# Optimization experiments

Measured on AMD Instinct MI355X. Metric: run time of the kernel, lower is better.

## Reference

```python
import jax, jax.numpy as jnp
import numpy as np

B, Hh, Ww, C = 32, 56, 56, 256
WIN, SHIFT, HEADS = 7, 3, 8
N = WIN * WIN
nW = (Hh // WIN) * (Ww // WIN)


def _rel_pos_index(w):
    coords = np.stack(np.meshgrid(np.arange(w), np.arange(w), indexing='ij'))  # (2,w,w)
    flat = coords.reshape(2, -1)
    rel = (flat[:, :, None] - flat[:, None, :]).transpose(1, 2, 0)  # (N,N,2)
    rel[..., 0] += w - 1
    rel[..., 1] += w - 1
    rel[..., 0] *= 2 * w - 1
    return rel.sum(-1)  # (N,N) int


def _shift_attn_mask(H, W, w, s):
    img = np.zeros((H, W))
    cnt = 0
    for hs in (slice(0, -w), slice(-w, -s), slice(-s, None)):
        for ws in (slice(0, -w), slice(-w, -s), slice(-s, None)):
            img[hs, ws] = cnt
            cnt += 1
    mw = img.reshape(H // w, w, W // w, w).transpose(0, 2, 1, 3).reshape(-1, w * w)  # (nW,N)
    diff = mw[:, None, :] - mw[:, :, None]
    return np.where(diff != 0, -100.0, 0.0).astype(np.float32)  # (nW,N,N)


REL_IDX = jnp.asarray(_rel_pos_index(WIN))


def layer_norm(x, g, b):
    m = x.mean(-1, keepdims=True)
    v = ((x - m) ** 2).mean(-1, keepdims=True)
    return (x - m) / jnp.sqrt(v + 1e-5) * g + b


def setup_inputs() -> dict:
    key = jax.random.key(0)
    ks = jax.random.split(key, 10)
    s02 = 0.02
    x = jax.random.normal(ks[0], (B, Hh * Ww, C), jnp.float32)
    qkv_w = jax.random.normal(ks[1], (3 * C, C), jnp.float32) * s02
    qkv_b = jnp.zeros((3 * C,), jnp.float32)
    rpb_table = jax.random.normal(ks[2], ((2 * WIN - 1) ** 2, HEADS), jnp.float32) * s02
    proj_w = jax.random.normal(ks[3], (C, C), jnp.float32) * s02
    proj_b = jnp.zeros((C,), jnp.float32)
    fc1_w = jax.random.normal(ks[4], (4 * C, C), jnp.float32) * s02
    fc1_b = jnp.zeros((4 * C,), jnp.float32)
    fc2_w = jax.random.normal(ks[5], (C, 4 * C), jnp.float32) * s02
    fc2_b = jnp.zeros((C,), jnp.float32)
    attn_mask = jnp.asarray(_shift_attn_mask(Hh, Ww, WIN, SHIFT))
    # saliency masks: per-token binary fg/bg -> additive 0/-100 key masks
    fg_tok = jax.random.bernoulli(ks[6], 0.5, (B * nW, N))
    sal_fg = jnp.where(fg_tok[:, None, :], 0.0, -100.0) * jnp.ones((1, N, 1), jnp.float32)
    sal_bg = jnp.where(fg_tok[:, None, :], -100.0, 0.0) * jnp.ones((1, N, 1), jnp.float32)
    return dict(x=x, qkv_w=qkv_w, qkv_b=qkv_b, rpb_table=rpb_table, proj_w=proj_w,
                proj_b=proj_b, norm1_g=jnp.ones((C,)), norm1_b=jnp.zeros((C,)),
                norm2_g=jnp.ones((C,)), norm2_b=jnp.zeros((C,)),
                fc1_w=fc1_w, fc1_b=fc1_b, fc2_w=fc2_w, fc2_b=fc2_b,
                attn_mask=attn_mask, sal_fg_attn_mask=sal_fg.astype(jnp.float32),
                sal_bg_attn_mask=sal_bg.astype(jnp.float32))


def reference(x, qkv_w, qkv_b, rpb_table, proj_w, proj_b, norm1_g, norm1_b,
              norm2_g, norm2_b, fc1_w, fc1_b, fc2_w, fc2_b,
              attn_mask, sal_fg_attn_mask, sal_bg_attn_mask):
    Bb, L, Cc = x.shape
    d = Cc // HEADS
    scale = d ** -0.5
    shortcut = x
    xn = layer_norm(x, norm1_g, norm1_b).reshape(Bb, Hh, Ww, Cc)
    xs = jnp.roll(xn, (-SHIFT, -SHIFT), axis=(1, 2))
    # window partition -> (B*nW, N, C)
    nh = Hh // WIN
    xw = xs.reshape(Bb, nh, WIN, nh, WIN, Cc).transpose(0, 1, 3, 2, 4, 5).reshape(-1, N, Cc)
    B_ = xw.shape[0]
    qkv = (xw @ qkv_w.T + qkv_b).reshape(B_, N, 3, HEADS, d).transpose(2, 0, 3, 1, 4)
    q, k, v = qkv[0] * scale, qkv[1], qkv[2]  # (B_, h, N, d)
    attn = jnp.einsum('bhnd,bhmd->bhnm', q, k)
    rpb = rpb_table[REL_IDX.reshape(-1)].reshape(N, N, HEADS).transpose(2, 0, 1)
    attn = attn + rpb[None]
    attn_fg = attn + sal_fg_attn_mask[:, None]
    attn_bg = attn + sal_bg_attn_mask[:, None]

    def add_shift(a):
        a = a.reshape(B_ // nW, nW, HEADS, N, N) + attn_mask[None, :, None]
        return a.reshape(B_, HEADS, N, N)

    p = jax.nn.softmax(add_shift(attn), axis=-1)
    p_fg = jax.nn.softmax(add_shift(attn_fg), axis=-1)
    p_bg = jax.nn.softmax(add_shift(attn_bg), axis=-1)
    o = jnp.einsum('bhnm,bhmd->bhnd', p + p_fg - p_bg, v)
    o = o.transpose(0, 2, 1, 3).reshape(B_, N, Cc)
    o = o @ proj_w.T + proj_b
    # window reverse + reverse shift
    xr = o.reshape(Bb, nh, nh, WIN, WIN, Cc).transpose(0, 1, 3, 2, 4, 5).reshape(Bb, Hh, Ww, Cc)
    xr = jnp.roll(xr, (SHIFT, SHIFT), axis=(1, 2)).reshape(Bb, L, Cc)
    x = shortcut + xr
    h = layer_norm(x, norm2_g, norm2_b)
    h = jax.nn.gelu(h @ fc1_w.T + fc1_b, approximate=False) @ fc2_w.T + fc2_b
    return x + h
```

## Files before the change

kernel.cpp:

```cpp
#include <hip/hip_runtime.h>
#include <hip/hip_bf16.h>

#define HH 56
#define WWD 56
#define WIN 7
#define SHIFT 3
#define HEADS 8
#define NTOK 49
#define NW 64
#define CDIM 256
#define DH 32
#define MROWS 100352
#define SCALE_Q 0.17677669529663687f

typedef float floatx4 __attribute__((ext_vector_type(4)));
typedef __bf16 bf16x8 __attribute__((ext_vector_type(8)));

__device__ __forceinline__ float wave_sum(float v) {
#pragma unroll
    for (int m = 1; m < 64; m <<= 1) v += __shfl_xor(v, m);
    return v;
}

__device__ __forceinline__ void glds16(const void* g, void* l) {
    __builtin_amdgcn_global_load_lds(
        (const __attribute__((address_space(1))) void*)g,
        (__attribute__((address_space(3))) void*)l, 16, 0, 0);
}

__global__ __launch_bounds__(256) void convert_weights_kernel(
    const float* __restrict__ qkv_w, const float* __restrict__ proj_w,
    const float* __restrict__ fc1_w, const float* __restrict__ fc2_w,
    __hip_bfloat16* __restrict__ dst)
{
    int i = blockIdx.x * 256 + threadIdx.x;
    float v;
    if (i < 196608)       v = qkv_w[i];
    else if (i < 262144)  v = proj_w[i - 196608];
    else if (i < 524288)  v = fc1_w[i - 262144];
    else                  v = fc2_w[i - 524288];
    dst[i] = __float2bfloat16(v);
}

template <bool SHIFTED>
__global__ __launch_bounds__(256) void ln_kernel(
    const float* __restrict__ x, const float* __restrict__ g,
    const float* __restrict__ bb, __hip_bfloat16* __restrict__ out)
{
    const int tok  = blockIdx.x * 4 + (threadIdx.x >> 6);
    const int lane = threadIdx.x & 63;
    const int c    = lane * 4;

    float4 v = *reinterpret_cast<const float4*>(x + (size_t)tok * CDIM + c);
    float s = v.x + v.y + v.z + v.w;
    s = wave_sum(s);
    const float mean = s * (1.0f / 256.0f);
    float d0 = v.x - mean, d1 = v.y - mean, d2 = v.z - mean, d3 = v.w - mean;
    float sq = d0 * d0 + d1 * d1 + d2 * d2 + d3 * d3;
    sq = wave_sum(sq);
    const float rstd = rsqrtf(sq * (1.0f / 256.0f) + 1e-5f);

    float4 gv = *reinterpret_cast<const float4*>(g + c);
    float4 bv = *reinterpret_cast<const float4*>(bb + c);

    union { __hip_bfloat16 h[4]; uint2 u; } pk;
    pk.h[0] = __float2bfloat16(d0 * rstd * gv.x + bv.x);
    pk.h[1] = __float2bfloat16(d1 * rstd * gv.y + bv.y);
    pk.h[2] = __float2bfloat16(d2 * rstd * gv.z + bv.z);
    pk.h[3] = __float2bfloat16(d3 * rstd * gv.w + bv.w);

    size_t oidx;
    if (SHIFTED) {
        int b = tok / 3136;
        int l = tok - b * 3136;
        int h = l / WWD, w = l - (l / WWD) * WWD;
        int hp = h - SHIFT; if (hp < 0) hp += HH;
        int wp = w - SHIFT; if (wp < 0) wp += WWD;
        int bwin = b * NW + (hp / WIN) * 8 + (wp / WIN);
        int n = (hp % WIN) * WIN + (wp % WIN);
        oidx = ((size_t)bwin * NTOK + n) * CDIM + c;
    } else {
        oidx = (size_t)tok * CDIM + c;
    }
    *reinterpret_cast<uint2*>(out + oidx) = pk.u;
}

template <int MODE>
__global__ __launch_bounds__(256) void gemm_kernel(
    const __hip_bfloat16* __restrict__ A,
    const __hip_bfloat16* __restrict__ Wt,
    const float* __restrict__ bias,
    void* __restrict__ outv,
    const float* __restrict__ aux,
    int M, int Nn, int K)
{
    __shared__ __hip_bfloat16 As[128 * 32];
    __shared__ __hip_bfloat16 Bs[128 * 32];

    const int t = threadIdx.x;
    const int wave = t >> 6, lane = t & 63;
    const int m0 = blockIdx.y * 128, n0 = blockIdx.x * 128;
    const int wr = (wave >> 1) * 64;
    const int wc = (wave & 1) * 64;

    floatx4 acc[4][4] = {};

    const int c0 = wave * 64 + lane;
    const int c1 = 256 + c0;
    const int r0 = c0 >> 2, p0 = c0 & 3, g0 = p0 ^ ((r0 >> 1) & 3);
    const int r1 = c1 >> 2, p1 = c1 & 3, g1 = p1 ^ ((r1 >> 1) & 3);
    const __hip_bfloat16* gA0 = A  + (size_t)(m0 + r0) * K + g0 * 8;
    const __hip_bfloat16* gA1 = A  + (size_t)(m0 + r1) * K + g1 * 8;
    const __hip_bfloat16* gB0 = Wt + (size_t)(n0 + r0) * K + g0 * 8;
    const __hip_bfloat16* gB1 = Wt + (size_t)(n0 + r1) * K + g1 * 8;
    const int base0 = (wave * 64) * 8;
    const int base1 = (256 + wave * 64) * 8;

    const int fm = lane & 15;
    const int g4 = lane >> 4;

    for (int k0 = 0; k0 < K; k0 += 32) {
        __syncthreads();
        glds16(gA0 + k0, As + base0);
        glds16(gA1 + k0, As + base1);
        glds16(gB0 + k0, Bs + base0);
        glds16(gB1 + k0, Bs + base1);
        __syncthreads();

        bf16x8 af[4], bfr[4];
#pragma unroll
        for (int mt = 0; mt < 4; ++mt) {
            const int ml = wr + mt * 16 + fm;
            af[mt] = *reinterpret_cast<const bf16x8*>(
                As + ml * 32 + ((g4 ^ ((ml >> 1) & 3)) * 8));
            const int nl = wc + mt * 16 + fm;
            bfr[mt] = *reinterpret_cast<const bf16x8*>(
                Bs + nl * 32 + ((g4 ^ ((nl >> 1) & 3)) * 8));
        }
#pragma unroll
        for (int mt = 0; mt < 4; ++mt)
#pragma unroll
            for (int nt = 0; nt < 4; ++nt)
                acc[mt][nt] = __builtin_amdgcn_mfma_f32_16x16x32_bf16(
                    af[mt], bfr[nt], acc[mt][nt], 0, 0, 0);
    }

    float bv[4];
#pragma unroll
    for (int nt = 0; nt < 4; ++nt) bv[nt] = bias[n0 + wc + nt * 16 + fm];

#pragma unroll
    for (int mt = 0; mt < 4; ++mt) {
#pragma unroll
        for (int r = 0; r < 4; ++r) {
            const int m_g = m0 + wr + mt * 16 + g4 * 4 + r;
            size_t row_idx = 0;
            if (MODE == 1) {
                int bwin = m_g / NTOK;
                int ntok = m_g - bwin * NTOK;
                int b = bwin >> 6, wi = bwin & 63;
                int rr = ntok / WIN, cc = ntok - rr * WIN;
                int hp = (wi >> 3) * WIN + rr;
                int wp = (wi & 7) * WIN + cc;
                int h = hp + SHIFT; if (h >= HH) h -= HH;
                int w = wp + SHIFT; if (w >= WWD) w -= WWD;
                row_idx = ((size_t)b * 3136 + h * WWD + w) * CDIM;
            }
#pragma unroll
            for (int nt = 0; nt < 4; ++nt) {
                const int n_g = n0 + wc + nt * 16 + fm;
                float val = acc[mt][nt][r] + bv[nt];
                if (MODE == 0) {
                    if (n_g < 256) val *= SCALE_Q;
                    reinterpret_cast<__hip_bfloat16*>(outv)[(size_t)m_g * Nn + n_g] =
                        __float2bfloat16(val);
                } else if (MODE == 2) {
                    float gl = 0.5f * val * (1.0f + erff(val * 0.70710678118654752f));
                    reinterpret_cast<__hip_bfloat16*>(outv)[(size_t)m_g * Nn + n_g] =
                        __float2bfloat16(gl);
                } else if (MODE == 3) {
                    size_t idx = (size_t)m_g * CDIM + n_g;
                    reinterpret_cast<float*>(outv)[idx] = aux[idx] + val;
                } else {
                    size_t idx = row_idx + n_g;
                    reinterpret_cast<float*>(outv)[idx] = aux[idx] + val;
                }
            }
        }
    }
}

__global__ __launch_bounds__(256) void attn_kernel(
    const __hip_bfloat16* __restrict__ qkv,
    const float* __restrict__ rpb_table,
    const float* __restrict__ sal_fg,
    __hip_bfloat16* __restrict__ o)
{
    __shared__ unsigned short Pl[4][64 * 64];
    __shared__ unsigned short Vt[4][32 * 64];
    __shared__ float rpb_l[4][172];

    const int t = threadIdx.x;
    const int wave = t >> 6, lane = t & 63;
    const int lane15 = lane & 15, g4 = lane >> 4;
    const int b_ = blockIdx.x >> 1;
    const int h = ((blockIdx.x & 1) << 2) | wave;

    unsigned short* Pw = Pl[wave];
    unsigned short* Vw = Vt[wave];
    float* rpbw = rpb_l[wave];

    const unsigned short* qkv_u = reinterpret_cast<const unsigned short*>(qkv);
    const size_t base = (size_t)b_ * (NTOK * 768) + h * DH;

#pragma unroll
    for (int it = 0; it < 32; ++it) {
        int idx = it * 64 + lane;
        int key = idx >> 5, d = idx & 31;
        unsigned short v = 0;
        if (key < NTOK) v = qkv_u[base + key * 768 + 512 + d];
        Vw[d * 64 + (((key >> 3) ^ (d & 7)) << 3) + (key & 7)] = v;
    }
#pragma unroll
    for (int it = 0; it < 3; ++it) {
        int i = it * 64 + lane;
        if (i < 169) rpbw[i] = rpb_table[i * 8 + h];
    }
    float sfv = (lane < NTOK) ? sal_fg[(size_t)b_ * (NTOK * NTOK) + lane] : -100.f;
    const unsigned long long fgmask = __ballot(sfv == 0.0f);

    bf16x8 kf[4], qf[4];
#pragma unroll
    for (int mt = 0; mt < 4; ++mt)
        kf[mt] = *reinterpret_cast<const bf16x8*>(
            qkv_u + base + (size_t)(mt * 16 + lane15) * 768 + 256 + g4 * 8);
#pragma unroll
    for (int nt = 0; nt < 4; ++nt)
        qf[nt] = *reinterpret_cast<const bf16x8*>(
            qkv_u + base + (size_t)(nt * 16 + lane15) * 768 + g4 * 8);

    floatx4 S[4][4] = {};
#pragma unroll
    for (int mt = 0; mt < 4; ++mt)
#pragma unroll
        for (int nt = 0; nt < 4; ++nt)
            S[mt][nt] = __builtin_amdgcn_mfma_f32_16x16x32_bf16(
                kf[mt], qf[nt], S[mt][nt], 0, 0, 0);

    const int wr_ = (b_ & 63) >> 3, wc_ = (b_ & 63) & 7;
    int qlin[4], qreg[4];
#pragma unroll
    for (int nt = 0; nt < 4; ++nt) {
        int q = nt * 16 + lane15;
        int qr = (q * 147) >> 10, qc = q - qr * 7;
        qlin[nt] = q + 6 * qr + 84;
        qreg[nt] = ((wr_ == 7) ? ((qr < 4) ? 1 : 2) : 0) * 3
                 + ((wc_ == 7) ? ((qc < 4) ? 1 : 2) : 0);
    }

#pragma unroll
    for (int mt = 0; mt < 4; ++mt)
#pragma unroll
        for (int r = 0; r < 4; ++r) {
            int key = mt * 16 + g4 * 4 + r;
            int kr = (key * 147) >> 10, kc = key - kr * 7;
            int klin = key + 6 * kr;
            int kreg = ((wr_ == 7) ? ((kr < 4) ? 1 : 2) : 0) * 3
                     + ((wc_ == 7) ? ((kc < 4) ? 1 : 2) : 0);
            bool pad = key >= NTOK;
#pragma unroll
            for (int nt = 0; nt < 4; ++nt) {
                int idx = qlin[nt] - klin;
                idx = idx < 0 ? 0 : (idx > 168 ? 168 : idx);
                float s = S[mt][nt][r] + rpbw[idx]
                        + ((qreg[nt] == kreg) ? 0.f : -100.f);
                S[mt][nt][r] = pad ? -1e30f : s;
            }
        }

    float M0[4], M1[4], M2[4], R0[4], R1[4], R2[4];
#pragma unroll
    for (int nt = 0; nt < 4; ++nt) {
        float a0 = -1e30f, a1 = -1e30f, a2 = -1e30f;
#pragma unroll
        for (int mt = 0; mt < 4; ++mt)
#pragma unroll
            for (int r = 0; r < 4; ++r) {
                int key = mt * 16 + g4 * 4 + r;
                float sf = ((fgmask >> key) & 1ULL) ? 0.f : -100.f;
                float s = S[mt][nt][r];
                a0 = fmaxf(a0, s);
                a1 = fmaxf(a1, s + sf);
                a2 = fmaxf(a2, s - 100.f - sf);
            }
        a0 = fmaxf(a0, __shfl_xor(a0, 16)); a0 = fmaxf(a0, __shfl_xor(a0, 32));
        a1 = fmaxf(a1, __shfl_xor(a1, 16)); a1 = fmaxf(a1, __shfl_xor(a1, 32));
        a2 = fmaxf(a2, __shfl_xor(a2, 16)); a2 = fmaxf(a2, __shfl_xor(a2, 32));
        float s0 = 0.f, s1 = 0.f, s2 = 0.f;
#pragma unroll
        for (int mt = 0; mt < 4; ++mt)
#pragma unroll
            for (int r = 0; r < 4; ++r) {
                int key = mt * 16 + g4 * 4 + r;
                float sf = ((fgmask >> key) & 1ULL) ? 0.f : -100.f;
                float s = S[mt][nt][r];
                s0 += __expf(s - a0);
                s1 += __expf(s + sf - a1);
                s2 += __expf(s - 100.f - sf - a2);
            }
        s0 += __shfl_xor(s0, 16); s0 += __shfl_xor(s0, 32);
        s1 += __shfl_xor(s1, 16); s1 += __shfl_xor(s1, 32);
        s2 += __shfl_xor(s2, 16); s2 += __shfl_xor(s2, 32);
        M0[nt] = a0; M1[nt] = a1; M2[nt] = a2;
        R0[nt] = 1.f / s0; R1[nt] = 1.f / s1; R2[nt] = 1.f / s2;
    }

#pragma unroll
    for (int mt = 0; mt < 4; ++mt)
#pragma unroll
        for (int rp = 0; rp < 2; ++rp) {
            int key0 = mt * 16 + g4 * 4 + 2 * rp;
            float sf0 = ((fgmask >> key0) & 1ULL) ? 0.f : -100.f;
            float sf1 = ((fgmask >> (key0 + 1)) & 1ULL) ? 0.f : -100.f;
            int chunk = key0 >> 3;
#pragma unroll
            for (int nt = 0; nt < 4; ++nt) {
                float sA = S[mt][nt][2 * rp];
                float sB = S[mt][nt][2 * rp + 1];
                float pA = __expf(sA - M0[nt]) * R0[nt]
                         + __expf(sA + sf0 - M1[nt]) * R1[nt]
                         - __expf(sA - 100.f - sf0 - M2[nt]) * R2[nt];
                float pB = __expf(sB - M0[nt]) * R0[nt]
                         + __expf(sB + sf1 - M1[nt]) * R1[nt]
                         - __expf(sB - 100.f - sf1 - M2[nt]) * R2[nt];
                union { __hip_bfloat16 hh[2]; unsigned u; } pk;
                pk.hh[0] = __float2bfloat16(pA);
                pk.hh[1] = __float2bfloat16(pB);
                int q = nt * 16 + lane15;
                int addr = q * 64 + ((chunk ^ (q & 7)) << 3) + (key0 & 7);
                *reinterpret_cast<unsigned*>(Pw + addr) = pk.u;
            }
        }

    floatx4 Oc[4][2] = {};
#pragma unroll
    for (int kc = 0; kc < 2; ++kc) {
        bf16x8 pa[4], vb[2];
#pragma unroll
        for (int mt = 0; mt < 4; ++mt) {
            int row = mt * 16 + lane15;
            pa[mt] = *reinterpret_cast<const bf16x8*>(
                Pw + row * 64 + (((kc * 4 + g4) ^ (row & 7)) << 3));
        }
#pragma unroll
        for (int n2 = 0; n2 < 2; ++n2) {
            int d = n2 * 16 + lane15;
            vb[n2] = *reinterpret_cast<const bf16x8*>(
                Vw + d * 64 + (((kc * 4 + g4) ^ (d & 7)) << 3));
        }
#pragma unroll
        for (int mt = 0; mt < 4; ++mt)
#pragma unroll
            for (int n2 = 0; n2 < 2; ++n2)
                Oc[mt][n2] = __builtin_amdgcn_mfma_f32_16x16x32_bf16(
                    pa[mt], vb[n2], Oc[mt][n2], 0, 0, 0);
    }

#pragma unroll
    for (int mt = 0; mt < 4; ++mt)
#pragma unroll
        for (int r = 0; r < 4; ++r) {
            int query = mt * 16 + g4 * 4 + r;
            if (query < NTOK) {
                __hip_bfloat16* op = o + ((size_t)b_ * NTOK + query) * CDIM + h * DH;
#pragma unroll
                for (int n2 = 0; n2 < 2; ++n2)
                    op[n2 * 16 + lane15] = __float2bfloat16(Oc[mt][n2][r]);
            }
        }
}

extern "C" void kernel_launch(void* const* d_in, const int* in_sizes, int n_in,
                              void* d_out, int out_size, void* d_ws, size_t ws_size,
                              hipStream_t stream)
{
    const float* x        = (const float*)d_in[0];
    const float* qkv_w    = (const float*)d_in[1];
    const float* qkv_b    = (const float*)d_in[2];
    const float* rpb_tab  = (const float*)d_in[3];
    const float* proj_w   = (const float*)d_in[4];
    const float* proj_b   = (const float*)d_in[5];
    const float* n1g      = (const float*)d_in[6];
    const float* n1b      = (const float*)d_in[7];
    const float* n2g      = (const float*)d_in[8];
    const float* n2b      = (const float*)d_in[9];
    const float* fc1_w    = (const float*)d_in[10];
    const float* fc1_b    = (const float*)d_in[11];
    const float* fc2_w    = (const float*)d_in[12];
    const float* fc2_b    = (const float*)d_in[13];
    const float* sal_fg   = (const float*)d_in[15];

    char* ws = (char*)d_ws;
    __hip_bfloat16* regA = (__hip_bfloat16*)ws;
    __hip_bfloat16* regB = (__hip_bfloat16*)(ws + 205520896);
    float*          x2   = (float*)(ws + 205520896 + 51380224);
    __hip_bfloat16* wbf  = (__hip_bfloat16*)(ws + 205520896 + 51380224 + 102760448);
    __hip_bfloat16* wqkv  = wbf;
    __hip_bfloat16* wproj = wbf + 196608;
    __hip_bfloat16* wfc1  = wbf + 262144;
    __hip_bfloat16* wfc2  = wbf + 524288;

    convert_weights_kernel<<<3072, 256, 0, stream>>>(qkv_w, proj_w, fc1_w, fc2_w, wbf);

    ln_kernel<true><<<MROWS / 4, 256, 0, stream>>>(x, n1g, n1b, regB);

    gemm_kernel<0><<<dim3(768 / 128, MROWS / 128), 256, 0, stream>>>(
        regB, wqkv, qkv_b, regA, nullptr, MROWS, 768, 256);

    attn_kernel<<<2048 * 2, 256, 0, stream>>>(regA, rpb_tab, sal_fg, regB);

    gemm_kernel<1><<<dim3(256 / 128, MROWS / 128), 256, 0, stream>>>(
        regB, wproj, proj_b, x2, x, MROWS, 256, 256);

    ln_kernel<false><<<MROWS / 4, 256, 0, stream>>>(x2, n2g, n2b, regB);

    gemm_kernel<2><<<dim3(1024 / 128, MROWS / 128), 256, 0, stream>>>(
        regB, wfc1, fc1_b, regA, nullptr, MROWS, 1024, 256);

    gemm_kernel<3><<<dim3(256 / 128, MROWS / 128), 256, 0, stream>>>(
        regA, wfc2, fc2_b, d_out, x2, MROWS, 256, 1024);
}
```

Measured before the change: 786.3 us.

## Collapse triple softmax into fg/bg partitioned exponentials with per-class coefficients

Rewrites the three softmaxes (plain, fg-masked, bg-masked) algebraically. Each score is exponentiated once against a per-class (fg or bg) max, and the combined probability p + p_fg - p_bg becomes that exponential times a per-row coefficient picked by the key's class. This cuts the transcendental count from about nine to one per score. The P tile is now staged in LDS in two 32-key halves with padded strides instead of an XOR swizzle, which shrinks LDS use, and V uses a padded transpose layout. The exp(-100) terms are kept exactly, but rounding differs slightly from the reference.

Result: faster. 721.3 us (-8.3%).

```diff
diff --git a/kernel.cpp b/kernel.cpp
--- a/kernel.cpp
+++ b/kernel.cpp
@@ -196,9 +196,9 @@
     const float* __restrict__ sal_fg,
     __hip_bfloat16* __restrict__ o)
 {
-    __shared__ unsigned short Pl[4][64 * 64];
-    __shared__ unsigned short Vt[4][32 * 64];
-    __shared__ float rpb_l[4][172];
+    __shared__ unsigned short Pl[4][64 * 40];
+    __shared__ unsigned short Vt[4][32 * 72];
+    __shared__ float rpb_l[4][176];
 
     const int t = threadIdx.x;
     const int wave = t >> 6, lane = t & 63;
@@ -217,9 +217,9 @@
     for (int it = 0; it < 32; ++it) {
         int idx = it * 64 + lane;
         int key = idx >> 5, d = idx & 31;
-        unsigned short v = 0;
-        if (key < NTOK) v = qkv_u[base + key * 768 + 512 + d];
-        Vw[d * 64 + (((key >> 3) ^ (d & 7)) << 3) + (key & 7)] = v;
+        unsigned short v = (key < NTOK) ? qkv_u[base + key * 768 + 512 + d]
+                                        : (unsigned short)0;
+        Vw[d * 72 + key] = v;
     }
 #pragma unroll
     for (int it = 0; it < 3; ++it) {
@@ -278,92 +278,88 @@
             }
         }
 
-    float M0[4], M1[4], M2[4], R0[4], R1[4], R2[4];
+    float Cfg[4], Cbg[4];
 #pragma unroll
     for (int nt = 0; nt < 4; ++nt) {
-        float a0 = -1e30f, a1 = -1e30f, a2 = -1e30f;
+        float mfg = -3e38f, mbg = -3e38f;
 #pragma unroll
         for (int mt = 0; mt < 4; ++mt)
 #pragma unroll
             for (int r = 0; r < 4; ++r) {
                 int key = mt * 16 + g4 * 4 + r;
-                float sf = ((fgmask >> key) & 1ULL) ? 0.f : -100.f;
+                bool fg = (fgmask >> key) & 1ULL;
                 float s = S[mt][nt][r];
-                a0 = fmaxf(a0, s);
-                a1 = fmaxf(a1, s + sf);
-                a2 = fmaxf(a2, s - 100.f - sf);
-            }
-        a0 = fmaxf(a0, __shfl_xor(a0, 16)); a0 = fmaxf(a0, __shfl_xor(a0, 32));
-        a1 = fmaxf(a1, __shfl_xor(a1, 16)); a1 = fmaxf(a1, __shfl_xor(a1, 32));
-        a2 = fmaxf(a2, __shfl_xor(a2, 16)); a2 = fmaxf(a2, __shfl_xor(a2, 32));
-        float s0 = 0.f, s1 = 0.f, s2 = 0.f;
+                mfg = fg ? fmaxf(mfg, s) : mfg;
+                mbg = fg ? mbg : fmaxf(mbg, s);
+            }
+        mfg = fmaxf(mfg, __shfl_xor(mfg, 16)); mfg = fmaxf(mfg, __shfl_xor(mfg, 32));
+        mbg = fmaxf(mbg, __shfl_xor(mbg, 16)); mbg = fmaxf(mbg, __shfl_xor(mbg, 32));
+        float t1 = 0.f, t2 = 0.f;
 #pragma unroll
         for (int mt = 0; mt < 4; ++mt)
 #pragma unroll
             for (int r = 0; r < 4; ++r) {
                 int key = mt * 16 + g4 * 4 + r;
-                float sf = ((fgmask >> key) & 1ULL) ? 0.f : -100.f;
-                float s = S[mt][nt][r];
-                s0 += __expf(s - a0);
-                s1 += __expf(s + sf - a1);
-                s2 += __expf(s - 100.f - sf - a2);
-            }
-        s0 += __shfl_xor(s0, 16); s0 += __shfl_xor(s0, 32);
-        s1 += __shfl_xor(s1, 16); s1 += __shfl_xor(s1, 32);
-        s2 += __shfl_xor(s2, 16); s2 += __shfl_xor(s2, 32);
-        M0[nt] = a0; M1[nt] = a1; M2[nt] = a2;
-        R0[nt] = 1.f / s0; R1[nt] = 1.f / s1; R2[nt] = 1.f / s2;
-    }
-
-#pragma unroll
-    for (int mt = 0; mt < 4; ++mt)
-#pragma unroll
-        for (int rp = 0; rp < 2; ++rp) {
-            int key0 = mt * 16 + g4 * 4 + 2 * rp;
-            float sf0 = ((fgmask >> key0) & 1ULL) ? 0.f : -100.f;
-            float sf1 = ((fgmask >> (key0 + 1)) & 1ULL) ? 0.f : -100.f;
-            int chunk = key0 >> 3;
-#pragma unroll
-            for (int nt = 0; nt < 4; ++nt) {
-                float sA = S[mt][nt][2 * rp];
-                float sB = S[mt][nt][2 * rp + 1];
-                float pA = __expf(sA - M0[nt]) * R0[nt]
-                         + __expf(sA + sf0 - M1[nt]) * R1[nt]
-                         - __expf(sA - 100.f - sf0 - M2[nt]) * R2[nt];
-                float pB = __expf(sB - M0[nt]) * R0[nt]
-                         + __expf(sB + sf1 - M1[nt]) * R1[nt]
-                         - __expf(sB - 100.f - sf1 - M2[nt]) * R2[nt];
-                union { __hip_bfloat16 hh[2]; unsigned u; } pk;
-                pk.hh[0] = __float2bfloat16(pA);
-                pk.hh[1] = __float2bfloat16(pB);
-                int q = nt * 16 + lane15;
-                int addr = q * 64 + ((chunk ^ (q & 7)) << 3) + (key0 & 7);
-                *reinterpret_cast<unsigned*>(Pw + addr) = pk.u;
+                bool fg = (fgmask >> key) & 1ULL;
+                float e = __expf(S[mt][nt][r] - (fg ? mfg : mbg));
+                S[mt][nt][r] = e;
+                t1 += fg ? e : 0.f;
+                t2 += fg ? 0.f : e;
+            }
+        t1 += __shfl_xor(t1, 16); t1 += __shfl_xor(t1, 32);
+        t2 += __shfl_xor(t2, 16); t2 += __shfl_xor(t2, 32);
+        const float m0 = fmaxf(mfg, mbg);
+        const float m1 = fmaxf(mfg, mbg - 100.f);
+        const float m2 = fmaxf(mfg - 100.f, mbg);
+        const float a1 = __expf(mfg - m0),          a2 = __expf(mbg - m0);
+        const float b1 = __expf(mfg - m1),          b2 = __expf(mbg - 100.f - m1);
+        const float c1 = __expf(mfg - 100.f - m2),  c2 = __expf(mbg - m2);
+        const float r0 = 1.f / (t1 * a1 + t2 * a2);
+        const float r1 = 1.f / (t1 * b1 + t2 * b2);
+        const float r2 = 1.f / (t1 * c1 + t2 * c2);
+        Cfg[nt] = a1 * r0 + b1 * r1 - c1 * r2;
+        Cbg[nt] = a2 * r0 + b2 * r1 - c2 * r2;
+    }
+
+    floatx4 Oc[4][2] = {};
+#pragma unroll
+    for (int kc = 0; kc < 2; ++kc) {
+#pragma unroll
+        for (int mh = 0; mh < 2; ++mh) {
+            const int mt = kc * 2 + mh;
+#pragma unroll
+            for (int rp = 0; rp < 2; ++rp) {
+                const int key0 = mt * 16 + g4 * 4 + 2 * rp;
+                const bool fg0 = (fgmask >> key0) & 1ULL;
+                const bool fg1 = (fgmask >> (key0 + 1)) & 1ULL;
+                const int keyLocal = key0 - kc * 32;
+#pragma unroll
+                for (int nt = 0; nt < 4; ++nt) {
+                    float pA = S[mt][nt][2 * rp]     * (fg0 ? Cfg[nt] : Cbg[nt]);
+                    float pB = S[mt][nt][2 * rp + 1] * (fg1 ? Cfg[nt] : Cbg[nt]);
+                    union { __hip_bfloat16 hh[2]; unsigned u; } pk;
+                    pk.hh[0] = __float2bfloat16(pA);
+                    pk.hh[1] = __float2bfloat16(pB);
+                    const int q = nt * 16 + lane15;
+                    *reinterpret_cast<unsigned*>(Pw + q * 40 + keyLocal) = pk.u;
+                }
             }
         }
-
-    floatx4 Oc[4][2] = {};
-#pragma unroll
-    for (int kc = 0; kc < 2; ++kc) {
         bf16x8 pa[4], vb[2];
 #pragma unroll
-        for (int mt = 0; mt < 4; ++mt) {
-            int row = mt * 16 + lane15;
-            pa[mt] = *reinterpret_cast<const bf16x8*>(
-                Pw + row * 64 + (((kc * 4 + g4) ^ (row & 7)) << 3));
-        }
-#pragma unroll
-        for (int n2 = 0; n2 < 2; ++n2) {
-            int d = n2 * 16 + lane15;
+        for (int mtile = 0; mtile < 4; ++mtile)
+            pa[mtile] = *reinterpret_cast<const bf16x8*>(
+                Pw + (mtile * 16 + lane15) * 40 + g4 * 8);
+#pragma unroll
+        for (int n2 = 0; n2 < 2; ++n2)
             vb[n2] = *reinterpret_cast<const bf16x8*>(
-                Vw + d * 64 + (((kc * 4 + g4) ^ (d & 7)) << 3));
-        }
-#pragma unroll
-        for (int mt = 0; mt < 4; ++mt)
+                Vw + (n2 * 16 + lane15) * 72 + kc * 32 + g4 * 8);
+#pragma unroll
+        for (int mtile = 0; mtile < 4; ++mtile)
 #pragma unroll
             for (int n2 = 0; n2 < 2; ++n2)
-                Oc[mt][n2] = __builtin_amdgcn_mfma_f32_16x16x32_bf16(
-                    pa[mt], vb[n2], Oc[mt][n2], 0, 0, 0);
+                Oc[mtile][n2] = __builtin_amdgcn_mfma_f32_16x16x32_bf16(
+                    pa[mtile], vb[n2], Oc[mtile][n2], 0, 0, 0);
     }
 
 #pragma unroll
```
